# Optimization experiments

Hardware: AMD Instinct MI355X
Metric: run time of the kernel (lower is better)

Reference implementation:

```python
import jax, jax.numpy as jnp
import numpy as np

MARGIN = 0.3
S = 15.0
LAMDA = 2.0

B, C = 8192, 10000


def setup_inputs() -> dict:
    key = jax.random.key(0)
    k1, k2 = jax.random.split(key)
    costh = jax.random.uniform(k1, (B, C), dtype=jnp.float32)  # cosine similarities
    label = jax.random.randint(k2, (B,), 0, C, dtype=jnp.int64)
    return {"costh": costh, "label": label}


def reference(costh, label):
    b = costh.shape[0]
    rows = jnp.arange(b)
    cos_t = costh[rows, label]                      # [B] target cosine
    delta = MARGIN * jnp.exp(1.0 - cos_t) / LAMDA   # [B] per-sample margin
    # subtract margin only at the target column, then scale
    logits = S * costh.at[rows, label].add(-delta)  # [B, C]
    logp = jax.nn.log_softmax(logits, axis=-1)
    loss = -jnp.mean(logp[rows, label])
    return loss
```

## Files before the change

### kernel.cpp

```cpp
#include <hip/hip_runtime.h>

#define MARGIN   0.3f
#define S_SCALE  15.0f
#define LAMDA    2.0f
#define NB       8192
#define NC       10000
#define MAXLOGIT 15.0f

__global__ __launch_bounds__(256) void dam_row_loss(const float* __restrict__ costh,
                                                    const int* __restrict__ label,
                                                    float* __restrict__ row_loss) {
    const int row = blockIdx.x;
    const int tid = threadIdx.x;
    const float* __restrict__ rowp = costh + (size_t)row * NC;

    float s = 0.0f;
    const float4* __restrict__ rp4 = (const float4*)rowp;
    const int n4 = NC / 4;
    for (int i = tid; i < n4; i += 256) {
        float4 v = rp4[i];
        s += __expf(fmaf(S_SCALE, v.x, -MAXLOGIT));
        s += __expf(fmaf(S_SCALE, v.y, -MAXLOGIT));
        s += __expf(fmaf(S_SCALE, v.z, -MAXLOGIT));
        s += __expf(fmaf(S_SCALE, v.w, -MAXLOGIT));
    }

    #pragma unroll
    for (int off = 32; off > 0; off >>= 1)
        s += __shfl_down(s, off, 64);
    __shared__ float wsum[4];
    if ((tid & 63) == 0) wsum[tid >> 6] = s;
    __syncthreads();

    if (tid == 0) {
        float tot = wsum[0] + wsum[1] + wsum[2] + wsum[3];
        const int lbl = label[row];
        const float cos_t = rowp[lbl];
        const float delta = (MARGIN / LAMDA) * __expf(1.0f - cos_t);
        const float t_logit = S_SCALE * (cos_t - delta);
        tot = tot - __expf(fmaf(S_SCALE, cos_t, -MAXLOGIT)) + __expf(t_logit - MAXLOGIT);
        const float lse = MAXLOGIT + __logf(tot);
        row_loss[row] = lse - t_logit;
    }
}

__global__ __launch_bounds__(256) void dam_reduce(const float* __restrict__ row_loss,
                                                  float* __restrict__ out) {
    const int tid = threadIdx.x;
    float s = 0.0f;
    for (int i = tid; i < NB; i += 256) s += row_loss[i];
    #pragma unroll
    for (int off = 32; off > 0; off >>= 1)
        s += __shfl_down(s, off, 64);
    __shared__ float wsum[4];
    if ((tid & 63) == 0) wsum[tid >> 6] = s;
    __syncthreads();
    if (tid == 0) out[0] = (wsum[0] + wsum[1] + wsum[2] + wsum[3]) * (1.0f / (float)NB);
}

extern "C" void kernel_launch(void* const* d_in, const int* in_sizes, int n_in,
                              void* d_out, int out_size, void* d_ws, size_t ws_size,
                              hipStream_t stream) {
    const float* costh = (const float*)d_in[0];
    const int*   label = (const int*)d_in[1];
    float* out = (float*)d_out;
    float* row_loss = (float*)d_ws;

    dam_row_loss<<<NB, 256, 0, stream>>>(costh, label, row_loss);
    dam_reduce<<<1, 256, 0, stream>>>(row_loss, out);
}
```

Before: 435.3 us.

## Assign one wavefront per row and fully unroll the row loop

Each 64-lane wavefront now handles a whole row, so a block covers four rows and there is no LDS reduction or __syncthreads. The 2500 float4 loads per row are fully unrolled (39 iterations plus a tail), which allows many loads in flight per lane. The label and target cosine are fetched at the start so that latency overlaps the streaming loop. The unrolled loop raises register pressure, and each wave serialises more work per row.

After: 436.0 us. About the same (+0.2%).

```diff
diff --git a/kernel.cpp b/kernel.cpp
--- a/kernel.cpp
+++ b/kernel.cpp
@@ -7,18 +7,29 @@
 #define NC       10000
 #define MAXLOGIT 15.0f
 
-__global__ __launch_bounds__(256) void dam_row_loss(const float* __restrict__ costh,
-                                                    const int* __restrict__ label,
-                                                    float* __restrict__ row_loss) {
-    const int row = blockIdx.x;
-    const int tid = threadIdx.x;
+__global__ __launch_bounds__(256, 4) void dam_row_loss(const float* __restrict__ costh,
+                                                       const int* __restrict__ label,
+                                                       float* __restrict__ row_loss) {
+    const int wave = threadIdx.x >> 6;
+    const int lane = threadIdx.x & 63;
+    const int row  = (blockIdx.x << 2) | wave;
     const float* __restrict__ rowp = costh + (size_t)row * NC;
+    const float4* __restrict__ rp4 = (const float4*)rowp;
+
+    const int lbl = label[row];
+    const float cos_t = rowp[lbl];
 
     float s = 0.0f;
-    const float4* __restrict__ rp4 = (const float4*)rowp;
-    const int n4 = NC / 4;
-    for (int i = tid; i < n4; i += 256) {
-        float4 v = rp4[i];
+    #pragma unroll
+    for (int j = 0; j < 39; ++j) {
+        float4 v = rp4[lane + (j << 6)];
+        s += __expf(fmaf(S_SCALE, v.x, -MAXLOGIT));
+        s += __expf(fmaf(S_SCALE, v.y, -MAXLOGIT));
+        s += __expf(fmaf(S_SCALE, v.z, -MAXLOGIT));
+        s += __expf(fmaf(S_SCALE, v.w, -MAXLOGIT));
+    }
+    if (lane < 4) {
+        float4 v = rp4[2496 + lane];
         s += __expf(fmaf(S_SCALE, v.x, -MAXLOGIT));
         s += __expf(fmaf(S_SCALE, v.y, -MAXLOGIT));
         s += __expf(fmaf(S_SCALE, v.z, -MAXLOGIT));
@@ -28,14 +39,9 @@
     #pragma unroll
     for (int off = 32; off > 0; off >>= 1)
         s += __shfl_down(s, off, 64);
-    __shared__ float wsum[4];
-    if ((tid & 63) == 0) wsum[tid >> 6] = s;
-    __syncthreads();
 
-    if (tid == 0) {
-        float tot = wsum[0] + wsum[1] + wsum[2] + wsum[3];
-        const int lbl = label[row];
-        const float cos_t = rowp[lbl];
+    if (lane == 0) {
+        float tot = s;
         const float delta = (MARGIN / LAMDA) * __expf(1.0f - cos_t);
         const float t_logit = S_SCALE * (cos_t - delta);
         tot = tot - __expf(fmaf(S_SCALE, cos_t, -MAXLOGIT)) + __expf(t_logit - MAXLOGIT);
@@ -48,6 +54,7 @@
                                                   float* __restrict__ out) {
     const int tid = threadIdx.x;
     float s = 0.0f;
+    #pragma unroll
     for (int i = tid; i < NB; i += 256) s += row_loss[i];
     #pragma unroll
     for (int off = 32; off > 0; off >>= 1)
@@ -66,6 +73,6 @@
     float* out = (float*)d_out;
     float* row_loss = (float*)d_ws;
 
-    dam_row_loss<<<NB, 256, 0, stream>>>(costh, label, row_loss);
+    dam_row_loss<<<NB / 4, 256, 0, stream>>>(costh, label, row_loss);
     dam_reduce<<<1, 256, 0, stream>>>(row_loss, out);
 }
```
